# Optimization experiments

Hardware: AMD Instinct MI355X
Metric: run time of the kernel (lower is better)

The kernel has to match this reference:

```python
import jax, jax.numpy as jnp
import numpy as np

NTOKENS = 50257
NHID = 1024
NTOK_PER_CLASS = 225   # ceil(sqrt(50257))
NCLASSES = 224         # ceil(50257/225)
BATCH = 2048


def setup_inputs() -> dict:
    key = jax.random.key(0)
    k1, k2, k3, k4 = jax.random.split(key, 4)
    initrange = 0.1
    inputs = jax.random.normal(k1, (BATCH, NHID), dtype=jnp.float32)
    labels = jax.random.randint(k2, (BATCH,), 0, NTOKENS, dtype=jnp.int64)
    layer_top_W = jax.random.uniform(k3, (NHID, NCLASSES), dtype=jnp.float32,
                                     minval=-initrange, maxval=initrange)
    layer_top_b = jnp.zeros((NCLASSES,), dtype=jnp.float32)
    layer_bottom_W = jax.random.uniform(k4, (NCLASSES, NHID, NTOK_PER_CLASS),
                                        dtype=jnp.float32,
                                        minval=-initrange, maxval=initrange)
    layer_bottom_b = jnp.zeros((NCLASSES, NTOK_PER_CLASS), dtype=jnp.float32)
    return {"inputs": inputs, "labels": labels,
            "layer_top_W": layer_top_W, "layer_top_b": layer_top_b,
            "layer_bottom_W": layer_bottom_W, "layer_bottom_b": layer_bottom_b}


def reference(inputs, labels, layer_top_W, layer_top_b, layer_bottom_W, layer_bottom_b):
    batch_size = inputs.shape[0]
    label_position_top = labels // NTOK_PER_CLASS          # [B]
    label_position_bottom = labels % NTOK_PER_CLASS        # [B]

    # top-level class probabilities
    top_logits = inputs @ layer_top_W + layer_top_b        # [B, nclasses]
    top_probs = jax.nn.softmax(top_logits, axis=1)

    # per-sample gather of class weight matrices + batched matmul
    W_sel = layer_bottom_W[label_position_top]             # [B, nhid, ntok_per_class]
    b_sel = layer_bottom_b[label_position_top]             # [B, ntok_per_class]
    bottom_logits = jnp.einsum('bh,bht->bt', inputs, W_sel) + b_sel
    bottom_probs = jax.nn.softmax(bottom_logits, axis=1)

    idx = jnp.arange(batch_size)
    target_probs = top_probs[idx, label_position_top] * bottom_probs[idx, label_position_bottom]
    return target_probs
```

## Files before the change

kernel.cpp:

```cpp
#include <hip/hip_runtime.h>
#include <math.h>

#define NHID  1024
#define NCLS  224
#define NTPC  225
#define BATCH 2048

#define KSPLIT 8
#define KCH    128
#define NTILES (BATCH / 16)
#define NBOT_BLOCKS (NCLS * KSPLIT)
#define NTOP_BLOCKS (NTILES * KSPLIT)

#define YTOPK (BATCH * NCLS)
#define YBOTK (BATCH * NTPC)

#define CLS_OFF  0
#define POS_OFF  8192
#define LIST_OFF 16384
#define OFFS_OFF 24576
#define YTOP_OFF 32768
#define YTOP_BYTES (KSPLIT * YTOPK * 4)
#define YBOT_OFF (YTOP_OFF + YTOP_BYTES)
#define YBOT_BYTES (KSPLIT * YBOTK * 4)

__global__ __launch_bounds__(256) void group_kernel(const int* __restrict__ labels,
                                                    int* __restrict__ cls,
                                                    int* __restrict__ pos,
                                                    int* __restrict__ list,
                                                    int* __restrict__ offs) {
    __shared__ int cnt[NCLS];
    __shared__ int sc[256];
    __shared__ int bex[NCLS];
    __shared__ int nz;
    const int tid = threadIdx.x;
    if (tid == 0) nz = 0;
    for (int j = tid; j < NCLS; j += 256) cnt[j] = 0;
    __syncthreads();
    int loc = 0;
    for (int k = 0; k < 4; ++k) {
        int i = tid + 256 * k;
        if (labels[2 * i + 1] != 0) loc = 1;
    }
    if (loc) atomicOr(&nz, 1);
    __syncthreads();
    const bool is64 = (nz == 0);
    int myc[8], myr[8];
#pragma unroll
    for (int k = 0; k < 8; ++k) {
        int i = tid + 256 * k;
        int l = is64 ? labels[2 * i] : labels[i];
        int c = l / NTPC;
        cls[i] = c;
        pos[i] = l - c * NTPC;
        myc[k] = c;
        myr[k] = atomicAdd(&cnt[c], 1);
    }
    __syncthreads();
    int v = (tid < NCLS) ? cnt[tid] : 0;
    sc[tid] = v;
    __syncthreads();
    for (int off = 1; off < 256; off <<= 1) {
        int u = (tid >= off) ? sc[tid - off] : 0;
        __syncthreads();
        sc[tid] += u;
        __syncthreads();
    }
    if (tid < NCLS) {
        int ex = sc[tid] - v;
        bex[tid] = ex;
        offs[tid] = ex;
    }
    if (tid == 0) offs[NCLS] = BATCH;
    __syncthreads();
#pragma unroll
    for (int k = 0; k < 8; ++k) {
        int i = tid + 256 * k;
        list[bex[myc[k]] + myr[k]] = i;
    }
}

template<int YC, bool BOT>
__device__ __forceinline__ void run_tiles(const float* __restrict__ x,
                                          const float* __restrict__ W,
                                          float* __restrict__ yk,
                                          const int* __restrict__ list,
                                          int o, int n, int hbase,
                                          float* __restrict__ xs) {
    const int tid = threadIdx.x;
    const int w = tid >> 6, l = tid & 63;
    const int col3  = 192 + l;
    const int col3c = min(col3, YC - 1);
    const int r  = tid & 127;
    const int hs = tid >> 7;
    const int rq = (r >> 1) & 3;
    const float4* xsq = (const float4*)xs;

    for (int tile = 0; tile * 16 < n; ++tile) {
        if (tile) __syncthreads();
        const float* xrow = x + hbase + r;
#pragma unroll
        for (int j = 0; j < 8; ++j) {
            const int i = hs * 8 + j;
            const int idx = tile * 16 + i;
            const int s = BOT ? list[o + min(idx, n - 1)] : (o + idx);
            xs[(r << 4) + ((((i >> 2) ^ rq) << 2) | (i & 3))] = xrow[(size_t)s * NHID];
        }
        __syncthreads();

        float acc[16];
#pragma unroll
        for (int i = 0; i < 16; ++i) acc[i] = 0.f;

        const float* wA = W + (size_t)hbase * YC + l;
        const float* w3 = W + (size_t)hbase * YC + col3c;

#pragma unroll 1
        for (int h0 = 0; h0 < KCH; h0 += 8) {
            const float* wB  = wA + 4 * YC;
            const float* w3B = w3 + 4 * YC;
#pragma unroll
            for (int j = 0; j < 8; ++j) {
                const float4 xv = xsq[(h0 + j) * 4 + (w ^ (j >> 1))];
                const float* wp  = (j < 4) ? wA : wB;
                const float* w3p = (j < 4) ? w3 : w3B;
                const int jj = j & 3;
                const float w0  = wp[jj * YC];
                const float w1  = wp[jj * YC + 64];
                const float w2  = wp[jj * YC + 128];
                const float w3v = w3p[jj * YC];
                acc[0]  = fmaf(xv.x, w0,  acc[0]);
                acc[1]  = fmaf(xv.x, w1,  acc[1]);
                acc[2]  = fmaf(xv.x, w2,  acc[2]);
                acc[3]  = fmaf(xv.x, w3v, acc[3]);
                acc[4]  = fmaf(xv.y, w0,  acc[4]);
                acc[5]  = fmaf(xv.y, w1,  acc[5]);
                acc[6]  = fmaf(xv.y, w2,  acc[6]);
                acc[7]  = fmaf(xv.y, w3v, acc[7]);
                acc[8]  = fmaf(xv.z, w0,  acc[8]);
                acc[9]  = fmaf(xv.z, w1,  acc[9]);
                acc[10] = fmaf(xv.z, w2,  acc[10]);
                acc[11] = fmaf(xv.z, w3v, acc[11]);
                acc[12] = fmaf(xv.w, w0,  acc[12]);
                acc[13] = fmaf(xv.w, w1,  acc[13]);
                acc[14] = fmaf(xv.w, w2,  acc[14]);
                acc[15] = fmaf(xv.w, w3v, acc[15]);
            }
            wA += 8 * YC;
            w3 += 8 * YC;
        }

        const int nt = min(n - tile * 16, 16);
#pragma unroll
        for (int jj = 0; jj < 4; ++jj) {
            const int it = 4 * w + jj;
            if (it < nt) {
                const int s = BOT ? list[o + tile * 16 + it] : (o + tile * 16 + it);
                float* yr = yk + (size_t)s * YC;
                yr[l]       = acc[jj * 4 + 0];
                yr[l + 64]  = acc[jj * 4 + 1];
                yr[l + 128] = acc[jj * 4 + 2];
                if (col3 < YC) yr[col3] = acc[jj * 4 + 3];
            }
        }
    }
}

__global__ __launch_bounds__(256, 8) void partial_kernel(const float* __restrict__ x,
                                                         const float* __restrict__ Wt,
                                                         const float* __restrict__ Wb,
                                                         const int* __restrict__ list,
                                                         const int* __restrict__ offs,
                                                         float* __restrict__ ytop,
                                                         float* __restrict__ ybot) {
    __shared__ __align__(16) float xs[KCH * 16];
    const int bi = blockIdx.x;
    if (bi < NBOT_BLOCKS) {
        const int c = bi % NCLS;
        const int k = bi / NCLS;
        const int o = offs[c];
        const int n = offs[c + 1] - o;
        run_tiles<NTPC, true>(x, Wb + (size_t)c * (NHID * NTPC),
                              ybot + (size_t)k * YBOTK, list, o, n, k * KCH, xs);
    } else {
        const int b2 = bi - NBOT_BLOCKS;
        const int st = b2 % NTILES;
        const int k  = b2 / NTILES;
        run_tiles<NCLS, false>(x, Wt, ytop + (size_t)k * YTOPK, list,
                               st * 16, 16, k * KCH, xs);
    }
}

__global__ __launch_bounds__(256) void finalize_kernel(const float* __restrict__ ytop,
                                                       const float* __restrict__ ybot,
                                                       const float* __restrict__ bt,
                                                       const float* __restrict__ bb,
                                                       const int* __restrict__ cls,
                                                       const int* __restrict__ pos,
                                                       float* __restrict__ out) {
    const int w = threadIdx.x >> 6, l = threadIdx.x & 63;
    const int s = blockIdx.x * 4 + w;
    const int c = cls[s], p = pos[s];

    float v[4];
#pragma unroll
    for (int g = 0; g < 4; ++g) {
        int col = l + 64 * g;
        if (col < NCLS) {
            float a = bt[col];
#pragma unroll
            for (int k = 0; k < KSPLIT; ++k)
                a += ytop[(size_t)k * YTOPK + (size_t)s * NCLS + col];
            v[g] = a;
        } else {
            v[g] = -INFINITY;
        }
    }
    float mx = fmaxf(fmaxf(v[0], v[1]), fmaxf(v[2], v[3]));
#pragma unroll
    for (int off = 32; off; off >>= 1) mx = fmaxf(mx, __shfl_xor(mx, off));
    float sum = 0.f, tc = 0.f;
#pragma unroll
    for (int g = 0; g < 4; ++g) {
        int col = l + 64 * g;
        float e = (col < NCLS) ? __expf(v[g] - mx) : 0.f;
        sum += e;
        if (col == c) tc = e;
    }
#pragma unroll
    for (int off = 32; off; off >>= 1) {
        sum += __shfl_xor(sum, off);
        tc  += __shfl_xor(tc, off);
    }
    const float tp = tc / sum;

#pragma unroll
    for (int g = 0; g < 4; ++g) {
        int col = l + 64 * g;
        if (col < NTPC) {
            float a = bb[c * NTPC + col];
#pragma unroll
            for (int k = 0; k < KSPLIT; ++k)
                a += ybot[(size_t)k * YBOTK + (size_t)s * NTPC + col];
            v[g] = a;
        } else {
            v[g] = -INFINITY;
        }
    }
    mx = fmaxf(fmaxf(v[0], v[1]), fmaxf(v[2], v[3]));
#pragma unroll
    for (int off = 32; off; off >>= 1) mx = fmaxf(mx, __shfl_xor(mx, off));
    float bsum = 0.f, ep = 0.f;
#pragma unroll
    for (int g = 0; g < 4; ++g) {
        int col = l + 64 * g;
        float e = (col < NTPC) ? __expf(v[g] - mx) : 0.f;
        bsum += e;
        if (col == p) ep = e;
    }
#pragma unroll
    for (int off = 32; off; off >>= 1) bsum += __shfl_xor(bsum, off);
#pragma unroll
    for (int g = 0; g < 4; ++g)
        if (l + 64 * g == p) out[s] = tp * ep / bsum;
}

extern "C" void kernel_launch(void* const* d_in, const int* in_sizes, int n_in,
                              void* d_out, int out_size, void* d_ws, size_t ws_size,
                              hipStream_t stream) {
    const float* inputs = (const float*)d_in[0];
    const int*   labels = (const int*)d_in[1];
    const float* topW   = (const float*)d_in[2];
    const float* topB   = (const float*)d_in[3];
    const float* botW   = (const float*)d_in[4];
    const float* botB   = (const float*)d_in[5];
    float* out = (float*)d_out;

    char* ws   = (char*)d_ws;
    int*   cls = (int*)(ws + CLS_OFF);
    int*   pos = (int*)(ws + POS_OFF);
    int*   lst = (int*)(ws + LIST_OFF);
    int*   off = (int*)(ws + OFFS_OFF);
    float* ytop = (float*)(ws + YTOP_OFF);
    float* ybot = (float*)(ws + YBOT_OFF);

    group_kernel<<<1, 256, 0, stream>>>(labels, cls, pos, lst, off);
    partial_kernel<<<NBOT_BLOCKS + NTOP_BLOCKS, 256, 0, stream>>>(
        inputs, topW, botW, lst, off, ytop, ybot);
    finalize_kernel<<<BATCH / 4, 256, 0, stream>>>(ytop, ybot, topB, botB, cls, pos, out);
}
```

Before: 351.5 us.

## Vectorize weight loads per thread with register double-buffering and padded partial outputs

Each thread now owns four contiguous output columns instead of four columns strided by 64. Weights are read with unaligned 16-byte vector loads, and the next 4-row group of weights is prefetched into registers while the current group is computed. The partial-sum buffers for the bottom level use a row stride padded to 228, so results can be written with aligned float4 stores, and the finalize kernel reads with the new strides. Launch bounds drop from 8 to 4 blocks per SM to give the extra prefetch registers room, at the cost of lower occupancy. The padded stride also enlarges the workspace.

Measured after the change: 333.8 us. 1.05x faster.

```diff
diff --git a/kernel.cpp b/kernel.cpp
--- a/kernel.cpp
+++ b/kernel.cpp
@@ -12,8 +12,10 @@
 #define NBOT_BLOCKS (NCLS * KSPLIT)
 #define NTOP_BLOCKS (NTILES * KSPLIT)
 
-#define YTOPK (BATCH * NCLS)
-#define YBOTK (BATCH * NTPC)
+#define YTS 224
+#define YBS 228
+#define YTOPK (BATCH * YTS)
+#define YBOTK (BATCH * YBS)
 
 #define CLS_OFF  0
 #define POS_OFF  8192
@@ -23,6 +25,8 @@
 #define YTOP_BYTES (KSPLIT * YTOPK * 4)
 #define YBOT_OFF (YTOP_OFF + YTOP_BYTES)
 #define YBOT_BYTES (KSPLIT * YBOTK * 4)
+
+typedef float f4u __attribute__((ext_vector_type(4), aligned(4)));
 
 __global__ __launch_bounds__(256) void group_kernel(const int* __restrict__ labels,
                                                     int* __restrict__ cls,
@@ -80,7 +84,7 @@
     }
 }
 
-template<int YC, bool BOT>
+template<int YC, int YS, bool BOT>
 __device__ __forceinline__ void run_tiles(const float* __restrict__ x,
                                           const float* __restrict__ W,
                                           float* __restrict__ yk,
@@ -89,8 +93,8 @@
                                           float* __restrict__ xs) {
     const int tid = threadIdx.x;
     const int w = tid >> 6, l = tid & 63;
-    const int col3  = 192 + l;
-    const int col3c = min(col3, YC - 1);
+    const int cb  = 4 * l;
+    const int cbc = min(cb, YC - 4);
     const int r  = tid & 127;
     const int hs = tid >> 7;
     const int rq = (r >> 1) & 3;
@@ -108,46 +112,53 @@
         }
         __syncthreads();
 
-        float acc[16];
-#pragma unroll
-        for (int i = 0; i < 16; ++i) acc[i] = 0.f;
-
-        const float* wA = W + (size_t)hbase * YC + l;
-        const float* w3 = W + (size_t)hbase * YC + col3c;
+        float4 acc[4];
+#pragma unroll
+        for (int i = 0; i < 4; ++i) acc[i] = make_float4(0.f, 0.f, 0.f, 0.f);
+
+        auto compute4 = [&](int hb, int ph, const f4u (&wv)[4]) {
+#pragma unroll
+            for (int j = 0; j < 4; ++j) {
+                const float4 xv = xsq[(hb + j) * 4 + (w ^ (ph + (j >> 1)))];
+                const f4u wq = wv[j];
+                acc[0].x = fmaf(xv.x, wq.x, acc[0].x);
+                acc[0].y = fmaf(xv.x, wq.y, acc[0].y);
+                acc[0].z = fmaf(xv.x, wq.z, acc[0].z);
+                acc[0].w = fmaf(xv.x, wq.w, acc[0].w);
+                acc[1].x = fmaf(xv.y, wq.x, acc[1].x);
+                acc[1].y = fmaf(xv.y, wq.y, acc[1].y);
+                acc[1].z = fmaf(xv.y, wq.z, acc[1].z);
+                acc[1].w = fmaf(xv.y, wq.w, acc[1].w);
+                acc[2].x = fmaf(xv.z, wq.x, acc[2].x);
+                acc[2].y = fmaf(xv.z, wq.y, acc[2].y);
+                acc[2].z = fmaf(xv.z, wq.z, acc[2].z);
+                acc[2].w = fmaf(xv.z, wq.w, acc[2].w);
+                acc[3].x = fmaf(xv.w, wq.x, acc[3].x);
+                acc[3].y = fmaf(xv.w, wq.y, acc[3].y);
+                acc[3].z = fmaf(xv.w, wq.z, acc[3].z);
+                acc[3].w = fmaf(xv.w, wq.w, acc[3].w);
+            }
+        };
+
+        const float* wp = W + (size_t)hbase * YC + cbc;
+        f4u wva[4], wvb[4];
+#pragma unroll
+        for (int j = 0; j < 4; ++j)
+            wva[j] = *(const f4u*)(wp + (size_t)j * YC);
 
 #pragma unroll 1
         for (int h0 = 0; h0 < KCH; h0 += 8) {
-            const float* wB  = wA + 4 * YC;
-            const float* w3B = w3 + 4 * YC;
-#pragma unroll
-            for (int j = 0; j < 8; ++j) {
-                const float4 xv = xsq[(h0 + j) * 4 + (w ^ (j >> 1))];
-                const float* wp  = (j < 4) ? wA : wB;
-                const float* w3p = (j < 4) ? w3 : w3B;
-                const int jj = j & 3;
-                const float w0  = wp[jj * YC];
-                const float w1  = wp[jj * YC + 64];
-                const float w2  = wp[jj * YC + 128];
-                const float w3v = w3p[jj * YC];
-                acc[0]  = fmaf(xv.x, w0,  acc[0]);
-                acc[1]  = fmaf(xv.x, w1,  acc[1]);
-                acc[2]  = fmaf(xv.x, w2,  acc[2]);
-                acc[3]  = fmaf(xv.x, w3v, acc[3]);
-                acc[4]  = fmaf(xv.y, w0,  acc[4]);
-                acc[5]  = fmaf(xv.y, w1,  acc[5]);
-                acc[6]  = fmaf(xv.y, w2,  acc[6]);
-                acc[7]  = fmaf(xv.y, w3v, acc[7]);
-                acc[8]  = fmaf(xv.z, w0,  acc[8]);
-                acc[9]  = fmaf(xv.z, w1,  acc[9]);
-                acc[10] = fmaf(xv.z, w2,  acc[10]);
-                acc[11] = fmaf(xv.z, w3v, acc[11]);
-                acc[12] = fmaf(xv.w, w0,  acc[12]);
-                acc[13] = fmaf(xv.w, w1,  acc[13]);
-                acc[14] = fmaf(xv.w, w2,  acc[14]);
-                acc[15] = fmaf(xv.w, w3v, acc[15]);
-            }
-            wA += 8 * YC;
-            w3 += 8 * YC;
+            const float* wpb = wp + 4 * (size_t)YC;
+#pragma unroll
+            for (int j = 0; j < 4; ++j)
+                wvb[j] = *(const f4u*)(wpb + (size_t)j * YC);
+            compute4(h0, 0, wva);
+            const float* wpa = wp + ((h0 + 8 < KCH) ? 8 : 0) * (size_t)YC;
+#pragma unroll
+            for (int j = 0; j < 4; ++j)
+                wva[j] = *(const f4u*)(wpa + (size_t)j * YC);
+            compute4(h0 + 4, 2, wvb);
+            wp += 8 * (size_t)YC;
         }
 
         const int nt = min(n - tile * 16, 16);
@@ -156,17 +167,18 @@
             const int it = 4 * w + jj;
             if (it < nt) {
                 const int s = BOT ? list[o + tile * 16 + it] : (o + tile * 16 + it);
-                float* yr = yk + (size_t)s * YC;
-                yr[l]       = acc[jj * 4 + 0];
-                yr[l + 64]  = acc[jj * 4 + 1];
-                yr[l + 128] = acc[jj * 4 + 2];
-                if (col3 < YC) yr[col3] = acc[jj * 4 + 3];
+                float* yr = yk + (size_t)s * YS;
+                if (cb + 3 < YC) {
+                    *(float4*)(yr + cb) = acc[jj];
+                } else if (cb < YC) {
+                    yr[cb] = acc[jj].w;
+                }
             }
         }
     }
 }
 
-__global__ __launch_bounds__(256, 8) void partial_kernel(const float* __restrict__ x,
+__global__ __launch_bounds__(256, 4) void partial_kernel(const float* __restrict__ x,
                                                          const float* __restrict__ Wt,
                                                          const float* __restrict__ Wb,
                                                          const int* __restrict__ list,
@@ -180,14 +192,14 @@
         const int k = bi / NCLS;
         const int o = offs[c];
         const int n = offs[c + 1] - o;
-        run_tiles<NTPC, true>(x, Wb + (size_t)c * (NHID * NTPC),
-                              ybot + (size_t)k * YBOTK, list, o, n, k * KCH, xs);
+        run_tiles<NTPC, YBS, true>(x, Wb + (size_t)c * (NHID * NTPC),
+                                   ybot + (size_t)k * YBOTK, list, o, n, k * KCH, xs);
     } else {
         const int b2 = bi - NBOT_BLOCKS;
         const int st = b2 % NTILES;
         const int k  = b2 / NTILES;
-        run_tiles<NCLS, false>(x, Wt, ytop + (size_t)k * YTOPK, list,
-                               st * 16, 16, k * KCH, xs);
+        run_tiles<NCLS, YTS, false>(x, Wt, ytop + (size_t)k * YTOPK, list,
+                                    st * 16, 16, k * KCH, xs);
     }
 }
 
@@ -210,7 +222,7 @@
             float a = bt[col];
 #pragma unroll
             for (int k = 0; k < KSPLIT; ++k)
-                a += ytop[(size_t)k * YTOPK + (size_t)s * NCLS + col];
+                a += ytop[(size_t)k * YTOPK + (size_t)s * YTS + col];
             v[g] = a;
         } else {
             v[g] = -INFINITY;
@@ -241,7 +253,7 @@
             float a = bb[c * NTPC + col];
 #pragma unroll
             for (int k = 0; k < KSPLIT; ++k)
-                a += ybot[(size_t)k * YBOTK + (size_t)s * NTPC + col];
+                a += ybot[(size_t)k * YBOTK + (size_t)s * YBS + col];
             v[g] = a;
         } else {
             v[g] = -INFINITY;
```
